# Kernel optimization log

Measured on AMD Instinct MI355X. Metric: run time of the kernel, lower is better.

## Reference

```python
import jax, jax.numpy as jnp
import numpy as np

# DNC dims: N memory slots, WM word size, R read heads, H controller hidden, D word_vec
N, WM, R, H, D = 256, 64, 4, 512, 512
T, B = 128, 32
EPS = 1e-6
IFACE = R*WM + R + WM + 1 + WM + WM + R + 1 + 1 + 3*R  # DNC interface vector size


def setup_inputs() -> dict:
    key = jax.random.key(0)
    k = jax.random.split(key, 8)
    in_dim = D + R*WM  # controller sees [x_t ; flattened read vectors]
    w = lambda kk, shape: jax.random.normal(kk, shape, jnp.float32) * 0.02
    return {
        "emb_utt": jax.random.normal(k[0], (T, B, D), jnp.float32),
        "Wx": w(k[1], (in_dim, 4*H)),
        "Wh": w(k[2], (H, 4*H)),
        "b_lstm": jnp.zeros((4*H,), jnp.float32),
        "W_pre": w(k[3], (H, D)),
        "b_pre": jnp.zeros((D,), jnp.float32),
        "W_iface": w(k[4], (H, IFACE)),
        "b_iface": jnp.zeros((IFACE,), jnp.float32),
        "W_rout": w(k[5], (R*WM, D)),
    }


def _content(M, keys, beta):
    # M: (B,N,WM); keys: (B,K,WM); beta: (B,K) -> content weighting (B,K,N)
    Mn = M / jnp.maximum(jnp.linalg.norm(M, axis=-1, keepdims=True), EPS)
    kn = keys / jnp.maximum(jnp.linalg.norm(keys, axis=-1, keepdims=True), EPS)
    sim = jnp.einsum('bkw,bnw->bkn', kn, Mn)
    return jax.nn.softmax(beta[..., None] * sim, axis=-1)


def _allocation(u):
    # usage-sort-based allocation weighting (Graves et al. 2016)
    idx = jnp.argsort(u, axis=1)  # ascending usage
    su = jnp.take_along_axis(u, idx, axis=1)
    excl = jnp.concatenate([jnp.ones_like(su[:, :1]), jnp.cumprod(su, axis=1)[:, :-1]], axis=1)
    a_sorted = (1.0 - su) * excl
    bidx = jnp.arange(u.shape[0])[:, None]
    return jnp.zeros_like(u).at[bidx, idx].set(a_sorted)


def reference(emb_utt, Wx, Wh, b_lstm, W_pre, b_pre, W_iface, b_iface, W_rout):
    Bsz = emb_utt.shape[1]
    eye = jnp.eye(N, dtype=emb_utt.dtype)

    def step(carry, x):
        h, c, M, usage, rw, ww, prec, link, rvec = carry
        # ---- controller (LSTM) ----
        xin = jnp.concatenate([x, rvec.reshape(Bsz, -1)], axis=1)
        gates = xin @ Wx + h @ Wh + b_lstm
        i, f, g, o = jnp.split(gates, 4, axis=1)
        c = jax.nn.sigmoid(f) * c + jax.nn.sigmoid(i) * jnp.tanh(g)
        h = jax.nn.sigmoid(o) * jnp.tanh(c)
        # ---- interface ----
        z = h @ W_iface + b_iface
        off = [0]
        def take(n):
            v = z[:, off[0]:off[0]+n]; off[0] += n; return v
        read_keys = take(R*WM).reshape(Bsz, R, WM)
        read_str = 1.0 + jax.nn.softplus(take(R))
        write_key = take(WM)
        write_str = 1.0 + jax.nn.softplus(take(1))
        erase = jax.nn.sigmoid(take(WM))
        write_vec = take(WM)
        free = jax.nn.sigmoid(take(R))
        alloc_g = jax.nn.sigmoid(take(1))
        write_g = jax.nn.sigmoid(take(1))
        modes = jax.nn.softmax(take(3*R).reshape(Bsz, R, 3), axis=-1)
        # ---- memory write ----
        retention = jnp.prod(1.0 - free[:, :, None] * rw, axis=1)   # (B,N)
        usage = (usage + ww - usage * ww) * retention
        alloc = _allocation(usage)
        cw = _content(M, write_key[:, None, :], write_str)[:, 0, :]  # (B,N)
        ww = write_g * (alloc_g * alloc + (1.0 - alloc_g) * cw)
        M = M * (1.0 - ww[:, :, None] * erase[:, None, :]) + ww[:, :, None] * write_vec[:, None, :]
        # temporal link matrix + precedence
        link = (1.0 - ww[:, :, None] - ww[:, None, :]) * link + ww[:, :, None] * prec[:, None, :]
        link = link * (1.0 - eye)
        prec = (1.0 - jnp.sum(ww, axis=1, keepdims=True)) * prec + ww
        # ---- memory read ----
        cr = _content(M, read_keys, read_str)                        # (B,R,N)
        fw = jnp.einsum('bij,brj->bri', link, rw)                    # forward
        bw = jnp.einsum('bji,brj->bri', link, rw)                    # backward
        rw = modes[..., 0:1] * bw + modes[..., 1:2] * cr + modes[..., 2:3] * fw
        rvec = jnp.einsum('brn,bnw->brw', rw, M)
        out = h @ W_pre + b_pre + rvec.reshape(Bsz, -1) @ W_rout
        return (h, c, M, usage, rw, ww, prec, link, rvec), out

    z = lambda *s: jnp.zeros(s, jnp.float32)
    carry0 = (z(Bsz, H), z(Bsz, H), jnp.full((Bsz, N, WM), EPS, jnp.float32),
              z(Bsz, N), z(Bsz, R, N), z(Bsz, N), z(Bsz, N),
              z(Bsz, N, N), z(Bsz, R, WM))
    _, outs = jax.lax.scan(step, carry0, emb_utt)
    return outs  # (T, B, D)
```

## Files before the change

### kernel.cpp

```cpp
#include <hip/hip_runtime.h>
#include <math.h>

#define TN   256
#define TWM  64
#define TR   4
#define TH   512
#define TD   512
#define TT   128
#define TB   32
#define IFACE 471
#define EPSI 1e-6f

#define OFF_H      0
#define OFF_C      32768
#define OFF_M      49152
#define OFF_USAGE  573440
#define OFF_RW     581632
#define OFF_WW     614400
#define OFF_PRECA  622592
#define OFF_LINK   638976
#define OFF_RVEC   2736128
#define OFF_MNORM  2744320
#define OFF_ZP     2752512
#define OFF_PARSE  2998272
#define OFF_CRS    3012608
#define OFF_FW     3045376
#define OFF_BWP    3078144
#define OFF_CNT    3340288
#define TOTAL_STATE 3340928

__device__ __forceinline__ float sigm(float x)  { return 1.0f / (1.0f + expf(-x)); }
__device__ __forceinline__ float softpl(float x){ return x > 20.0f ? x : log1pf(expf(x)); }

__device__ __forceinline__ float ldc(const float* p) {
    return __hip_atomic_load(p, __ATOMIC_RELAXED, __HIP_MEMORY_SCOPE_AGENT);
}
__device__ __forceinline__ void stc(float* p, float v) {
    __hip_atomic_store(p, v, __ATOMIC_RELAXED, __HIP_MEMORY_SCOPE_AGENT);
}
__device__ __forceinline__ void stcv4(float* p, float4 v) {
    stc(p, v.x); stc(p + 1, v.y); stc(p + 2, v.z); stc(p + 3, v.w);
}

__global__ void k_init(float* ws) {
    int idx = blockIdx.x * 256 + threadIdx.x;
    if (idx >= TOTAL_STATE) return;
    float v = 0.0f;
    if (idx >= OFF_M && idx < OFF_M + TB*TN*TWM) v = EPSI;
    if (idx >= OFF_MNORM && idx < OFF_MNORM + TB*TN) v = 8e-6f;
    ws[idx] = v;
}

__device__ __forceinline__ void out_phase(
    const float* __restrict__ W_pre, const float* __restrict__ b_pre,
    const float* __restrict__ W_rout, const float* __restrict__ ws,
    float* __restrict__ out, float* sm, const int tid, const int B2, const int t)
{
    float* act_s = sm;
    float* red_s = sm + 3072;
    const int q = B2 >> 5, s = (B2 >> 3) & 3, bg = B2 & 7, b0 = bg * 4;
    for (int i = tid; i < 768; i += 512) {
        const int bb = i / 192;
        const int k0 = (i - bb*192) * 4;
        const float* src = (k0 < 512) ? &ws[OFF_H + (t&1)*(TB*TH) + (b0+bb)*TH + k0]
                                      : &ws[OFF_RVEC + (b0+bb)*256 + (k0 - 512)];
        *(float4*)&act_s[bb*768 + k0] = *(const float4*)src;
    }
    __syncthreads();
    const int c0 = q*128 + s*32;
    const int col = tid & 31;
    const int ksb = tid >> 5;
    float a0=0, a1=0, a2=0, a3=0;
    for (int kk = ksb*48; kk < ksb*48 + 48; ++kk) {
        const float w = (kk < 512) ? W_pre[(size_t)kk * 512 + c0 + col]
                                   : W_rout[(size_t)(kk - 512) * 512 + c0 + col];
        a0 += act_s[kk]        * w;
        a1 += act_s[768 + kk]  * w;
        a2 += act_s[1536 + kk] * w;
        a3 += act_s[2304 + kk] * w;
    }
    red_s[(ksb*4 + 0)*32 + col] = a0;
    red_s[(ksb*4 + 1)*32 + col] = a1;
    red_s[(ksb*4 + 2)*32 + col] = a2;
    red_s[(ksb*4 + 3)*32 + col] = a3;
    __syncthreads();
    if (tid < 128) {
        const int cc = tid & 31, bb = tid >> 5;
        float ssum = 0.0f;
        #pragma unroll
        for (int ks2 = 0; ks2 < 16; ++ks2) ssum += red_s[(ks2*4 + bb)*32 + cc];
        ssum += b_pre[c0 + cc];
        out[(size_t)(t - 1) * (TB * TD) + (b0+bb) * TD + c0 + cc] = ssum;
    }
}

__global__ __launch_bounds__(512) void k_front(
    const float* __restrict__ emb, const float* __restrict__ Wx,
    const float* __restrict__ Wh,  const float* __restrict__ b_lstm,
    const float* __restrict__ W_pre, const float* __restrict__ b_pre,
    const float* __restrict__ W_rout,
    float* __restrict__ ws, float* __restrict__ out, int t)
{
    __shared__ __align__(16) float smem[16384];
    const int tid = threadIdx.x;
    if (blockIdx.x >= 128) {
        if (t == 0) return;
        const int raw2 = blockIdx.x - 128;
        const int B2 = (((raw2 >> 2) & 3) << 5) | ((raw2 & 3) << 3) | (raw2 >> 4);
        out_phase(W_pre, b_pre, W_rout, ws, out, smem, tid, B2, t);
        return;
    }
    if (t >= TT) return;

    const int ublk = ((blockIdx.x & 7) << 4) | (blockIdx.x >> 3);
    const int u0  = ublk * 4;
    const int cg  = tid & 3;
    const int bg  = (tid >> 2) & 7;
    const int ks  = tid >> 5;
    const int col0 = cg * 512 + u0;
    const float* hbuf = ws + OFF_H + (t & 1) * (TB * TH);

    float acc[4][4] = {};

    for (int tile = 0; tile < 5; ++tile) {
        const int T0 = tile * 256;
        {
            const int b = tid & 31, kf4 = tid >> 5;
            #pragma unroll
            for (int i = 0; i < 4; ++i) {
                const int kf = kf4 * 4 + i;
                const int kl = kf * 4;
                const int k  = T0 + kl;
                const float* src;
                if (k < 512)      src = emb + (size_t)t * (TB*TD) + b * TD + k;
                else if (k < 768) src = ws + OFF_RVEC + b * 256 + (k - 512);
                else              src = hbuf + b * TH + (k - 768);
                float4 v = *(const float4*)src;
                smem[(kl+0)*32 + b] = v.x;
                smem[(kl+1)*32 + b] = v.y;
                smem[(kl+2)*32 + b] = v.z;
                smem[(kl+3)*32 + b] = v.w;
            }
        }
        __syncthreads();
        {
            const int k0 = T0 + ks * 16;
            const float* wp = (k0 < 768 ? Wx + (size_t)k0 * 2048
                                        : Wh + (size_t)(k0 - 768) * 2048) + col0;
            const float* ap = &smem[(ks * 16) * 32 + bg * 4];
            #pragma unroll 8
            for (int kk = 0; kk < 16; ++kk) {
                float4 wv = *(const float4*)wp; wp += 2048;
                float4 av = *(const float4*)ap; ap += 32;
                acc[0][0] += wv.x*av.x; acc[0][1] += wv.x*av.y; acc[0][2] += wv.x*av.z; acc[0][3] += wv.x*av.w;
                acc[1][0] += wv.y*av.x; acc[1][1] += wv.y*av.y; acc[1][2] += wv.y*av.z; acc[1][3] += wv.y*av.w;
                acc[2][0] += wv.z*av.x; acc[2][1] += wv.z*av.y; acc[2][2] += wv.z*av.z; acc[2][3] += wv.z*av.w;
                acc[3][0] += wv.w*av.x; acc[3][1] += wv.w*av.y; acc[3][2] += wv.w*av.z; acc[3][3] += wv.w*av.w;
            }
        }
        __syncthreads();
    }

    {
        const int rbase = 8192 + ks * 512 + (cg * 8 + bg) * 16;
        *(float4*)&smem[rbase + 0]  = make_float4(acc[0][0], acc[0][1], acc[0][2], acc[0][3]);
        *(float4*)&smem[rbase + 4]  = make_float4(acc[1][0], acc[1][1], acc[1][2], acc[1][3]);
        *(float4*)&smem[rbase + 8]  = make_float4(acc[2][0], acc[2][1], acc[2][2], acc[2][3]);
        *(float4*)&smem[rbase + 12] = make_float4(acc[3][0], acc[3][1], acc[3][2], acc[3][3]);
    }
    __syncthreads();
    {
        const int o = tid;
        float s = 0.0f;
        #pragma unroll
        for (int kq = 0; kq < 16; ++kq) s += smem[8192 + kq * 512 + o];
        const int ocg = o >> 7, obg = (o >> 4) & 7, odu = (o >> 2) & 3, obb = o & 3;
        s += b_lstm[ocg * 512 + u0 + odu];
        smem[(ocg * 4 + odu) * 32 + (obg * 4 + obb)] = s;
    }
    __syncthreads();
    if (tid < 128) {
        const int du = tid >> 5, b = tid & 31;
        const float ig = smem[(0  + du) * 32 + b];
        const float fg = smem[(4  + du) * 32 + b];
        const float gg = smem[(8  + du) * 32 + b];
        const float og = smem[(12 + du) * 32 + b];
        const int ci = b * TH + u0 + du;
        const float cold = ws[OFF_C + ci];
        const float cn = sigm(fg) * cold + sigm(ig) * tanhf(gg);
        const float hn = sigm(og) * tanhf(cn);
        ws[OFF_C + ci] = cn;
        ws[OFF_H + ((t + 1) & 1) * (TB * TH) + ci] = hn;
    }
}

__device__ void stepA_fn(const float* __restrict__ b_if, float* __restrict__ ws,
                         const int t, const int b, const int tid, float* sm)
{
    float* z_s      = sm + 0;
    float* rwf_s    = sm + 480;
    float* ww_old_s = sm + 1504;
    float* ww_s     = sm + 1760;
    float* u_s      = sm + 2016;
    float* prec_s   = sm + 2272;
    float* mnorm_s  = sm + 2528;
    float* alloc_s  = sm + 2784;
    float* cw_s     = sm + 3040;
    float* keysp    = sm + 3296;
    float* wkey_s   = sm + 3552;
    float* erase_s  = sm + 3616;
    float* wvec_s   = sm + 3680;
    float* rstr_s   = sm + 3744;
    float* free_s   = sm + 3748;
    float* modesp   = sm + 3752;
    float* knorm_s  = sm + 3764;
    float* sredA_s  = sm + 3772;
    float* sc_s     = sm + 3780;
    float* Pt_s     = sm + 3788;

    const float* wsM = ws + OFF_M + b * (TN * TWM);
    const float* precOld = ws + OFF_PRECA + (t & 1) * (TB * TN) + b * 256;
    float* precNew = ws + OFF_PRECA + ((t + 1) & 1) * (TB * TN) + b * 256;

    if (tid < 256)       { *(float4*)&rwf_s[tid*4] = *(const float4*)&ws[OFF_RW + b*1024 + tid*4]; }
    else if (tid < 320)  { const int i = tid-256; *(float4*)&ww_old_s[i*4] = *(const float4*)&ws[OFF_WW + b*256 + i*4]; }
    else if (tid < 384)  { const int i = tid-320; *(float4*)&u_s[i*4]      = *(const float4*)&ws[OFF_USAGE + b*256 + i*4]; }
    else if (tid < 448)  { const int i = tid-384; *(float4*)&prec_s[i*4]   = *(const float4*)&precOld[i*4]; }
    else                 { const int i = tid-448; *(float4*)&mnorm_s[i*4]  = *(const float4*)&ws[OFF_MNORM + b*256 + i*4]; }
    if (tid < IFACE) {
        float part[16];
        #pragma unroll
        for (int p = 0; p < 16; ++p)
            part[p] = ldc(&ws[OFF_ZP + ((size_t)p*32 + b) * 480 + tid]);
        float zv = b_if[tid];
        #pragma unroll
        for (int p = 0; p < 16; ++p) zv += part[p];
        z_s[tid] = zv;
    }
    __syncthreads();

    if (tid < IFACE) {
        const float v = z_s[tid];
        if (tid < 256)       keysp[(tid >> 6)*64 + (tid & 63)] = v;
        else if (tid < 260)  rstr_s[tid - 256] = 1.0f + softpl(v);
        else if (tid < 324)  wkey_s[tid - 260] = v;
        else if (tid == 324) sc_s[0] = 1.0f + softpl(v);
        else if (tid < 389)  erase_s[tid - 325] = sigm(v);
        else if (tid < 453)  wvec_s[tid - 389] = v;
        else if (tid < 457)  free_s[tid - 453] = sigm(v);
        else if (tid == 457) sc_s[1] = sigm(v);
        else if (tid == 458) sc_s[2] = sigm(v);
    }
    __syncthreads();
    if (tid < 320) {
        const int w5 = tid >> 6, lane = tid & 63;
        const float v = (w5 == 0) ? wkey_s[lane] : keysp[(w5 - 1)*64 + lane];
        float s = v * v;
        #pragma unroll
        for (int m = 1; m <= 32; m <<= 1) s += __shfl_xor(s, m);
        if (lane == 0) knorm_s[w5] = fmaxf(sqrtf(s), EPSI);
    } else if (tid >= 508) {
        const int r = tid - 508;
        const float m0 = z_s[459 + r*3], m1 = z_s[460 + r*3], m2 = z_s[461 + r*3];
        const float mx = fmaxf(m0, fmaxf(m1, m2));
        const float e0 = expf(m0 - mx), e1 = expf(m1 - mx), e2 = expf(m2 - mx);
        const float s = e0 + e1 + e2;
        modesp[r*3+0] = e0 / s; modesp[r*3+1] = e1 / s; modesp[r*3+2] = e2 / s;
    }
    __syncthreads();

    if (tid < 404) {
        float v;
        if (tid < 256)       v = keysp[tid];
        else if (tid < 320)  v = erase_s[tid - 256];
        else if (tid < 384)  v = wvec_s[tid - 320];
        else if (tid < 388)  v = rstr_s[tid - 384];
        else if (tid < 392)  v = knorm_s[tid - 388 + 1];
        else                 v = modesp[tid - 392];
        ws[OFF_PARSE + b * 448 + tid] = v;
    }
    if (tid < 256) {
        float ret = 1.0f;
        #pragma unroll
        for (int r = 0; r < 4; ++r) ret *= 1.0f - free_s[r] * rwf_s[r*256 + tid];
        const float un = (u_s[tid] + ww_old_s[tid] - u_s[tid] * ww_old_s[tid]) * ret;
        u_s[tid] = un;
        ws[OFF_USAGE + b * 256 + tid] = un;
    }
    __syncthreads();

    {
        const int q = tid >> 8, n = tid & 255;
        const float un = u_s[n];
        float p = 1.0f;
        #pragma unroll 8
        for (int m = q * 128; m < q * 128 + 128; ++m) {
            const float um = u_s[m];
            const bool lt = (um < un) || (um == un && m < n);
            p *= lt ? um : 1.0f;
        }
        Pt_s[q * 256 + n] = p;
    }
    __syncthreads();
    if (tid < 256)
        alloc_s[tid] = (1.0f - u_s[tid]) * Pt_s[tid] * Pt_s[256 + tid];
    __syncthreads();

    {
        const int n = tid >> 1, q2 = tid & 1;
        const float* mp = wsM + n * 64 + q2 * 32;
        float s = 0.0f;
        #pragma unroll
        for (int it = 0; it < 8; ++it) {
            float4 mv = *(const float4*)(mp + it * 4);
            float4 kv = *(const float4*)&wkey_s[q2 * 32 + it * 4];
            s += mv.x*kv.x + mv.y*kv.y + mv.z*kv.z + mv.w*kv.w;
        }
        s += __shfl_xor(s, 1);
        if (q2 == 0) cw_s[n] = sc_s[0] * s / (knorm_s[0] * mnorm_s[n]);
    }
    __syncthreads();
    {
        float v = 0.0f, e = 0.0f;
        if (tid < 256) {
            v = cw_s[tid];
            float m = v;
            #pragma unroll
            for (int mm = 1; mm <= 32; mm <<= 1) m = fmaxf(m, __shfl_xor(m, mm));
            if ((tid & 63) == 0) sredA_s[tid >> 6] = m;
        }
        __syncthreads();
        if (tid == 0) sc_s[4] = fmaxf(fmaxf(sredA_s[0], sredA_s[1]), fmaxf(sredA_s[2], sredA_s[3]));
        __syncthreads();
        if (tid < 256) {
            e = expf(v - sc_s[4]);
            float s2 = e;
            #pragma unroll
            for (int mm = 1; mm <= 32; mm <<= 1) s2 += __shfl_xor(s2, mm);
            if ((tid & 63) == 0) sredA_s[tid >> 6] = s2;
        }
        __syncthreads();
        if (tid == 0) sc_s[5] = sredA_s[0] + sredA_s[1] + sredA_s[2] + sredA_s[3];
        __syncthreads();
        if (tid < 256) cw_s[tid] = e / sc_s[5];
    }
    __syncthreads();

    if (tid < 256) {
        const float wwn = sc_s[2] * (sc_s[1] * alloc_s[tid] + (1.0f - sc_s[1]) * cw_s[tid]);
        ww_s[tid] = wwn;
        ws[OFF_WW + b * 256 + tid] = wwn;
    }
    __syncthreads();
    if (tid < 256) {
        float s = ww_s[tid];
        #pragma unroll
        for (int mm = 1; mm <= 32; mm <<= 1) s += __shfl_xor(s, mm);
        if ((tid & 63) == 0) sredA_s[tid >> 6] = s;
    }
    __syncthreads();
    if (tid == 0) sc_s[3] = sredA_s[0] + sredA_s[1] + sredA_s[2] + sredA_s[3];
    __syncthreads();
    if (tid < 256)
        precNew[tid] = (1.0f - sc_s[3]) * prec_s[tid] + ww_s[tid];
}

__global__ __launch_bounds__(512) void k_zpA(
    const float* __restrict__ W_if, const float* __restrict__ b_if,
    float* __restrict__ ws, int t)
{
    __shared__ __align__(16) float h1_s[128];
    __shared__ __align__(16) float smA[4304];
    __shared__ int myBatch;
    const int tid = threadIdx.x;
    const int raw = blockIdx.x;
    const int bgz = raw >> 4;
    const int q = (raw >> 2) & 3, s = raw & 3;
    const int b0 = bgz * 4;

    if (tid < 128) {
        const int bb = tid >> 5, kk = tid & 31;
        h1_s[bb*32 + kk] = ws[OFF_H + ((t+1)&1)*(TB*TH) + (b0+bb)*TH + q*128 + s*32 + kk];
    }
    __syncthreads();
    if (tid < IFACE) {
        const int col = tid;
        float a0=0, a1=0, a2=0, a3=0;
        const float* wb = W_if + (size_t)(q*128 + s*32) * IFACE + col;
        #pragma unroll 8
        for (int kk = 0; kk < 32; ++kk) {
            const float w = *wb; wb += IFACE;
            a0 += h1_s[kk]      * w;
            a1 += h1_s[32+kk]   * w;
            a2 += h1_s[64+kk]   * w;
            a3 += h1_s[96+kk]   * w;
        }
        const size_t base = OFF_ZP + ((size_t)(q*4+s)*32 + b0) * 480 + col;
        stc(&ws[base],        a0);
        stc(&ws[base + 480],  a1);
        stc(&ws[base + 960],  a2);
        stc(&ws[base + 1440], a3);
    }
    asm volatile("s_waitcnt vmcnt(0)" ::: "memory");
    __syncthreads();
    if (tid == 0) {
        unsigned* cnt = (unsigned*)(ws + OFF_CNT) + bgz * 16;
        const unsigned old = __hip_atomic_fetch_add(cnt, 1u, __ATOMIC_RELAXED, __HIP_MEMORY_SCOPE_AGENT);
        const unsigned base = 16u * (unsigned)t;
        int mb = -1;
        if (old >= base + 12u) {
            mb = b0 + (int)(old - (base + 12u));
            while (__hip_atomic_load(cnt, __ATOMIC_RELAXED, __HIP_MEMORY_SCOPE_AGENT) < base + 16u)
                __builtin_amdgcn_s_sleep(2);
        }
        myBatch = mb;
    }
    __syncthreads();
    if (myBatch < 0) return;
    stepA_fn(b_if, ws, t, myBatch, tid, smA);
}

__device__ void stepB_fn(float* __restrict__ ws, const int t, const int b,
                         const int tid, float* sm)
{
    float* crp     = sm;
    float* rw2_s   = sm + 1024;
    float* Lt2     = sm + 2048;
    float* md      = sm + 4096;
    float* sredA_s = sm + 4112;
    float* sredB_s = sm + 4120;
    float* gmax_s  = sm + 4128;
    float* gsum_s  = sm + 4132;
    const float* wsM = ws + OFF_M + b * (TN * TWM);

    crp[tid]       = ldc(&ws[OFF_CRS + b*1024 + tid]);
    crp[tid + 512] = ldc(&ws[OFF_CRS + b*1024 + tid + 512]);
    if (tid < 12) md[tid] = ws[OFF_PARSE + b*448 + 392 + tid];
    __syncthreads();

    {
        const int rr = tid >> 8, n = tid & 255, wv = tid >> 6, lane = tid & 63;
        float v0 = crp[rr*256 + n], v1 = crp[(rr + 2)*256 + n];
        float m0 = v0, m1 = v1;
        #pragma unroll
        for (int mm = 1; mm <= 32; mm <<= 1) {
            m0 = fmaxf(m0, __shfl_xor(m0, mm));
            m1 = fmaxf(m1, __shfl_xor(m1, mm));
        }
        if (lane == 0) { sredA_s[wv] = m0; sredB_s[wv] = m1; }
        __syncthreads();
        if (tid < 4) {
            const float* base = (tid & 2) ? sredB_s : sredA_s;
            const int off = (tid & 1) * 4;
            gmax_s[tid] = fmaxf(fmaxf(base[off], base[off+1]), fmaxf(base[off+2], base[off+3]));
        }
        __syncthreads();
        const float e0 = expf(v0 - gmax_s[rr]);
        const float e1 = expf(v1 - gmax_s[rr + 2]);
        float s0 = e0, s1 = e1;
        #pragma unroll
        for (int mm = 1; mm <= 32; mm <<= 1) {
            s0 += __shfl_xor(s0, mm); s1 += __shfl_xor(s1, mm);
        }
        if (lane == 0) { sredA_s[wv] = s0; sredB_s[wv] = s1; }
        __syncthreads();
        if (tid < 4) {
            const float* base = (tid & 2) ? sredB_s : sredA_s;
            const int off = (tid & 1) * 4;
            gsum_s[tid] = base[off] + base[off+1] + base[off+2] + base[off+3];
        }
        __syncthreads();
        crp[rr*256 + n]       = e0 / gsum_s[rr];
        crp[(rr + 2)*256 + n] = e1 / gsum_s[rr + 2];
    }
    __syncthreads();

    {
        const int rr = tid >> 8, n = tid & 255;
        #pragma unroll
        for (int p = 0; p < 2; ++p) {
            const int r = rr + 2 * p;
            float part[8];
            #pragma unroll
            for (int c = 0; c < 8; ++c)
                part[c] = ldc(&ws[OFF_BWP + (size_t)(b*8 + c)*1024 + r*256 + n]);
            const float fwv = ldc(&ws[OFF_FW + b*1024 + r*256 + n]);
            float bw = 0.0f;
            #pragma unroll
            for (int c = 0; c < 8; ++c) bw += part[c];
            const float v = md[r*3] * bw + md[r*3+1] * crp[r*256 + n] + md[r*3+2] * fwv;
            rw2_s[r*256 + n] = v;
            ws[OFF_RW + b*1024 + r*256 + n] = v;
        }
    }
    __syncthreads();

    {
        const int g8 = tid >> 6, w = tid & 63;
        float p0=0, p1=0, p2=0, p3=0;
        const float* mb = wsM + (size_t)(g8 * 32) * 64 + w;
        for (int gg = 0; gg < 4; ++gg) {
            float mv[8];
            #pragma unroll
            for (int j = 0; j < 8; ++j) mv[j] = ldc(mb + (gg*8 + j) * 64);
            #pragma unroll
            for (int j = 0; j < 8; ++j) {
                const int n = g8*32 + gg*8 + j;
                p0 += rw2_s[n]       * mv[j];
                p1 += rw2_s[256 + n] * mv[j];
                p2 += rw2_s[512 + n] * mv[j];
                p3 += rw2_s[768 + n] * mv[j];
            }
        }
        Lt2[(g8*4 + 0)*64 + w] = p0;
        Lt2[(g8*4 + 1)*64 + w] = p1;
        Lt2[(g8*4 + 2)*64 + w] = p2;
        Lt2[(g8*4 + 3)*64 + w] = p3;
    }
    __syncthreads();
    if (tid < 256) {
        const int r = tid >> 6, w = tid & 63;
        float s = 0.0f;
        #pragma unroll
        for (int g = 0; g < 8; ++g) s += Lt2[(g*4 + r)*64 + w];
        ws[OFF_RVEC + b * 256 + tid] = s;
    }
}

__global__ __launch_bounds__(512) void k_linkB(float* __restrict__ ws, int t)
{
    __shared__ __align__(16) float sml[10272];
    __shared__ int isTail;
    float* ww_s   = sml;
    float* prec_s = sml + 256;
    float* rw_s   = sml + 512;
    float* pk_s   = sml + 1536;
    float* Lt     = sml + 2048;

    const int bi = blockIdx.x;
    const int b  = bi >> 3;
    const int c  = bi & 7;
    const int tid = threadIdx.x;
    const float* precOld = ws + OFF_PRECA + (t & 1) * (TB * TN) + b * 256;

    if (tid < 64)        { *(float4*)&ww_s[tid*4] = *(const float4*)&ws[OFF_WW + b*256 + tid*4]; }
    else if (tid < 128)  { const int i = tid-64;  *(float4*)&prec_s[i*4] = *(const float4*)&precOld[i*4]; }
    else if (tid < 384)  { const int i = tid-128; *(float4*)&rw_s[i*4]   = *(const float4*)&ws[OFF_RW + b*1024 + i*4]; }
    else if (tid < 496)  { const int i = tid-384; *(float4*)&pk_s[i*4]   = *(const float4*)&ws[OFF_PARSE + b*448 + i*4]; }
    __syncthreads();

    {
        const int ric = tid >> 4, c4 = (tid & 15) * 4;
        const int gi  = c * 32 + ric;
        float* mp = ws + OFF_M + b * (TN*TWM) + gi * 64 + c4;
        float4 m = *(const float4*)mp;
        const float wwi = ww_s[gi];
        float4 er = *(const float4*)&pk_s[256 + c4];
        float4 wv = *(const float4*)&pk_s[320 + c4];
        m.x = m.x * (1.0f - wwi * er.x) + wwi * wv.x;
        m.y = m.y * (1.0f - wwi * er.y) + wwi * wv.y;
        m.z = m.z * (1.0f - wwi * er.z) + wwi * wv.z;
        m.w = m.w * (1.0f - wwi * er.w) + wwi * wv.w;
        stcv4(mp, m);
        float sn = m.x*m.x + m.y*m.y + m.z*m.z + m.w*m.w;
        float d0 = m.x*pk_s[c4]     + m.y*pk_s[c4+1]     + m.z*pk_s[c4+2]     + m.w*pk_s[c4+3];
        float d1 = m.x*pk_s[64+c4]  + m.y*pk_s[64+c4+1]  + m.z*pk_s[64+c4+2]  + m.w*pk_s[64+c4+3];
        float d2 = m.x*pk_s[128+c4] + m.y*pk_s[128+c4+1] + m.z*pk_s[128+c4+2] + m.w*pk_s[128+c4+3];
        float d3 = m.x*pk_s[192+c4] + m.y*pk_s[192+c4+1] + m.z*pk_s[192+c4+2] + m.w*pk_s[192+c4+3];
        #pragma unroll
        for (int mm = 1; mm <= 8; mm <<= 1) {
            sn += __shfl_xor(sn, mm);
            d0 += __shfl_xor(d0, mm); d1 += __shfl_xor(d1, mm);
            d2 += __shfl_xor(d2, mm); d3 += __shfl_xor(d3, mm);
        }
        if ((tid & 15) == 0) {
            const float mn = fmaxf(sqrtf(sn), EPSI);
            ws[OFF_MNORM + b*256 + gi] = mn;
            const float inv = 1.0f / mn;
            stc(&ws[OFF_CRS + b*1024 + 0*256 + gi], pk_s[384+0] * d0 * inv / pk_s[388+0]);
            stc(&ws[OFF_CRS + b*1024 + 1*256 + gi], pk_s[384+1] * d1 * inv / pk_s[388+1]);
            stc(&ws[OFF_CRS + b*1024 + 2*256 + gi], pk_s[384+2] * d2 * inv / pk_s[388+2]);
            stc(&ws[OFF_CRS + b*1024 + 3*256 + gi], pk_s[384+3] * d3 * inv / pk_s[388+3]);
        }
    }

    {
        const int j = tid & 255, p = tid >> 8;
        const float wwj = ww_s[j], pj = prec_s[j];
        #pragma unroll 4
        for (int it = 0; it < 16; ++it) {
            const int ric = it * 2 + p;
            const int gi  = c * 32 + ric;
            float* lp = ws + OFF_LINK + (size_t)b * (TN*TN) + (size_t)gi * 256 + j;
            const float wwi = ww_s[gi];
            float v = (1.0f - wwi - wwj) * (*lp) + wwi * pj;
            if (j == gi) v = 0.0f;
            *lp = v;
            Lt[ric * 257 + j] = v;
        }
    }
    __syncthreads();

    {
        const int ric = tid >> 4, g = tid & 15;
        const int gi = c * 32 + ric;
        float f0=0, f1=0, f2=0, f3=0;
        #pragma unroll 4
        for (int jj = 0; jj < 16; ++jj) {
            const int j = g * 16 + jj;
            const float v = Lt[ric * 257 + j];
            f0 += v * rw_s[j]; f1 += v * rw_s[256+j];
            f2 += v * rw_s[512+j]; f3 += v * rw_s[768+j];
        }
        #pragma unroll
        for (int mm = 1; mm <= 8; mm <<= 1) {
            f0 += __shfl_xor(f0, mm); f1 += __shfl_xor(f1, mm);
            f2 += __shfl_xor(f2, mm); f3 += __shfl_xor(f3, mm);
        }
        if (g == 0) {
            stc(&ws[OFF_FW + b*1024 + gi],       f0);
            stc(&ws[OFF_FW + b*1024 + 256 + gi], f1);
            stc(&ws[OFF_FW + b*1024 + 512 + gi], f2);
            stc(&ws[OFF_FW + b*1024 + 768 + gi], f3);
        }
    }

    {
        const int j = tid & 255, p = tid >> 8;
        float b0=0, b1=0, b2=0, b3=0;
        #pragma unroll 4
        for (int it = 0; it < 16; ++it) {
            const int ric = p * 16 + it;
            const int gi  = c * 32 + ric;
            const float v = Lt[ric * 257 + j];
            b0 += v * rw_s[gi]; b1 += v * rw_s[256+gi];
            b2 += v * rw_s[512+gi]; b3 += v * rw_s[768+gi];
        }
        __syncthreads();
        if (p == 1) { Lt[j] = b0; Lt[256+j] = b1; Lt[512+j] = b2; Lt[768+j] = b3; }
        __syncthreads();
        if (p == 0) {
            stc(&ws[OFF_BWP + (size_t)bi*1024 + j],       b0 + Lt[j]);
            stc(&ws[OFF_BWP + (size_t)bi*1024 + 256 + j], b1 + Lt[256+j]);
            stc(&ws[OFF_BWP + (size_t)bi*1024 + 512 + j], b2 + Lt[512+j]);
            stc(&ws[OFF_BWP + (size_t)bi*1024 + 768 + j], b3 + Lt[768+j]);
        }
    }

    asm volatile("s_waitcnt vmcnt(0)" ::: "memory");
    __syncthreads();
    if (tid == 0) {
        unsigned* cnt = (unsigned*)(ws + OFF_CNT) + (8 + b) * 16;
        const unsigned old = __hip_atomic_fetch_add(cnt, 1u, __ATOMIC_RELAXED, __HIP_MEMORY_SCOPE_AGENT);
        isTail = (old == 8u * (unsigned)t + 7u) ? 1 : 0;
    }
    __syncthreads();
    if (!isTail) return;
    stepB_fn(ws, t, b, tid, sml);
}

extern "C" void kernel_launch(void* const* d_in, const int* in_sizes, int n_in,
                              void* d_out, int out_size, void* d_ws, size_t ws_size,
                              hipStream_t stream) {
    const float* emb    = (const float*)d_in[0];
    const float* Wx     = (const float*)d_in[1];
    const float* Wh     = (const float*)d_in[2];
    const float* b_lstm = (const float*)d_in[3];
    const float* W_pre  = (const float*)d_in[4];
    const float* b_pre  = (const float*)d_in[5];
    const float* W_if   = (const float*)d_in[6];
    const float* b_if   = (const float*)d_in[7];
    const float* W_rout = (const float*)d_in[8];
    float* out = (float*)d_out;
    float* ws  = (float*)d_ws;

    k_init<<<(TOTAL_STATE + 255) / 256, 256, 0, stream>>>(ws);
    for (int t = 0; t < TT; ++t) {
        k_front<<<256, 512, 0, stream>>>(emb, Wx, Wh, b_lstm, W_pre, b_pre, W_rout, ws, out, t);
        k_zpA<<<128, 512, 0, stream>>>(W_if, b_if, ws, t);
        k_linkB<<<256, 512, 0, stream>>>(ws, t);
    }
    k_front<<<256, 512, 0, stream>>>(emb, Wx, Wh, b_lstm, W_pre, b_pre, W_rout, ws, out, TT);
}
```

Baseline: 7.467 ms.

## Fuse interface and link kernels into one launch with per-batch flag sync

Merges the interface/stepA kernel and the link/memory-update kernel into a single 256-block kernel per timestep. Link blocks now spin on a per-batch flag that the stepA tail block sets, instead of waiting on a kernel boundary. The aim is to drop one launch per step (128 per run) and let batches proceed independently. The cost is a dependence on all 256 blocks being co-resident to avoid deadlock, plus spin-wait overhead and extra atomic loads and stores.

```diff
diff --git a/kernel.cpp b/kernel.cpp
--- a/kernel.cpp
+++ b/kernel.cpp
@@ -27,7 +27,11 @@
 #define OFF_FW     3045376
 #define OFF_BWP    3078144
 #define OFF_CNT    3340288
-#define TOTAL_STATE 3340928
+#define TOTAL_STATE 3341440
+
+#define CNT_ZPG(g) (OFF_CNT + (g)*16)
+#define CNT_SB(b)  (OFF_CNT + (8+(b))*16)
+#define CNT_FA(b)  (OFF_CNT + (40+(b))*16)
 
 __device__ __forceinline__ float sigm(float x)  { return 1.0f / (1.0f + expf(-x)); }
 __device__ __forceinline__ float softpl(float x){ return x > 20.0f ? x : log1pf(expf(x)); }
@@ -37,6 +41,11 @@
 }
 __device__ __forceinline__ void stc(float* p, float v) {
     __hip_atomic_store(p, v, __ATOMIC_RELAXED, __HIP_MEMORY_SCOPE_AGENT);
+}
+__device__ __forceinline__ float4 ldcv4(const float* p) {
+    float4 v;
+    v.x = ldc(p); v.y = ldc(p + 1); v.z = ldc(p + 2); v.w = ldc(p + 3);
+    return v;
 }
 __device__ __forceinline__ void stcv4(float* p, float4 v) {
     stc(p, v.x); stc(p + 1, v.y); stc(p + 2, v.z); stc(p + 3, v.w);
@@ -277,7 +286,7 @@
         else if (tid < 388)  v = rstr_s[tid - 384];
         else if (tid < 392)  v = knorm_s[tid - 388 + 1];
         else                 v = modesp[tid - 392];
-        ws[OFF_PARSE + b * 448 + tid] = v;
+        stc(&ws[OFF_PARSE + b * 448 + tid], v);
     }
     if (tid < 256) {
         float ret = 1.0f;
@@ -349,7 +358,7 @@
     if (tid < 256) {
         const float wwn = sc_s[2] * (sc_s[1] * alloc_s[tid] + (1.0f - sc_s[1]) * cw_s[tid]);
         ww_s[tid] = wwn;
-        ws[OFF_WW + b * 256 + tid] = wwn;
+        stc(&ws[OFF_WW + b * 256 + tid], wwn);
     }
     __syncthreads();
     if (tid < 256) {
@@ -363,61 +372,6 @@
     __syncthreads();
     if (tid < 256)
         precNew[tid] = (1.0f - sc_s[3]) * prec_s[tid] + ww_s[tid];
-}
-
-__global__ __launch_bounds__(512) void k_zpA(
-    const float* __restrict__ W_if, const float* __restrict__ b_if,
-    float* __restrict__ ws, int t)
-{
-    __shared__ __align__(16) float h1_s[128];
-    __shared__ __align__(16) float smA[4304];
-    __shared__ int myBatch;
-    const int tid = threadIdx.x;
-    const int raw = blockIdx.x;
-    const int bgz = raw >> 4;
-    const int q = (raw >> 2) & 3, s = raw & 3;
-    const int b0 = bgz * 4;
-
-    if (tid < 128) {
-        const int bb = tid >> 5, kk = tid & 31;
-        h1_s[bb*32 + kk] = ws[OFF_H + ((t+1)&1)*(TB*TH) + (b0+bb)*TH + q*128 + s*32 + kk];
-    }
-    __syncthreads();
-    if (tid < IFACE) {
-        const int col = tid;
-        float a0=0, a1=0, a2=0, a3=0;
-        const float* wb = W_if + (size_t)(q*128 + s*32) * IFACE + col;
-        #pragma unroll 8
-        for (int kk = 0; kk < 32; ++kk) {
-            const float w = *wb; wb += IFACE;
-            a0 += h1_s[kk]      * w;
-            a1 += h1_s[32+kk]   * w;
-            a2 += h1_s[64+kk]   * w;
-            a3 += h1_s[96+kk]   * w;
-        }
-        const size_t base = OFF_ZP + ((size_t)(q*4+s)*32 + b0) * 480 + col;
-        stc(&ws[base],        a0);
-        stc(&ws[base + 480],  a1);
-        stc(&ws[base + 960],  a2);
-        stc(&ws[base + 1440], a3);
-    }
-    asm volatile("s_waitcnt vmcnt(0)" ::: "memory");
-    __syncthreads();
-    if (tid == 0) {
-        unsigned* cnt = (unsigned*)(ws + OFF_CNT) + bgz * 16;
-        const unsigned old = __hip_atomic_fetch_add(cnt, 1u, __ATOMIC_RELAXED, __HIP_MEMORY_SCOPE_AGENT);
-        const unsigned base = 16u * (unsigned)t;
-        int mb = -1;
-        if (old >= base + 12u) {
-            mb = b0 + (int)(old - (base + 12u));
-            while (__hip_atomic_load(cnt, __ATOMIC_RELAXED, __HIP_MEMORY_SCOPE_AGENT) < base + 16u)
-                __builtin_amdgcn_s_sleep(2);
-        }
-        myBatch = mb;
-    }
-    __syncthreads();
-    if (myBatch < 0) return;
-    stepA_fn(b_if, ws, t, myBatch, tid, smA);
 }
 
 __device__ void stepB_fn(float* __restrict__ ws, const int t, const int b,
@@ -435,7 +389,7 @@
 
     crp[tid]       = ldc(&ws[OFF_CRS + b*1024 + tid]);
     crp[tid + 512] = ldc(&ws[OFF_CRS + b*1024 + tid + 512]);
-    if (tid < 12) md[tid] = ws[OFF_PARSE + b*448 + 392 + tid];
+    if (tid < 12) md[tid] = ldc(&ws[OFF_PARSE + b*448 + 392 + tid]);
     __syncthreads();
 
     {
@@ -527,136 +481,202 @@
     }
 }
 
-__global__ __launch_bounds__(512) void k_linkB(float* __restrict__ ws, int t)
+__global__ __launch_bounds__(512) void k_step(
+    const float* __restrict__ W_if, const float* __restrict__ b_if,
+    float* __restrict__ ws, int t)
 {
-    __shared__ __align__(16) float sml[10272];
+    __shared__ __align__(16) float sm[10272];
+    __shared__ int myBatch;
     __shared__ int isTail;
-    float* ww_s   = sml;
-    float* prec_s = sml + 256;
-    float* rw_s   = sml + 512;
-    float* pk_s   = sml + 1536;
-    float* Lt     = sml + 2048;
-
-    const int bi = blockIdx.x;
-    const int b  = bi >> 3;
-    const int c  = bi & 7;
     const int tid = threadIdx.x;
-    const float* precOld = ws + OFF_PRECA + (t & 1) * (TB * TN) + b * 256;
-
-    if (tid < 64)        { *(float4*)&ww_s[tid*4] = *(const float4*)&ws[OFF_WW + b*256 + tid*4]; }
-    else if (tid < 128)  { const int i = tid-64;  *(float4*)&prec_s[i*4] = *(const float4*)&precOld[i*4]; }
-    else if (tid < 384)  { const int i = tid-128; *(float4*)&rw_s[i*4]   = *(const float4*)&ws[OFF_RW + b*1024 + i*4]; }
-    else if (tid < 496)  { const int i = tid-384; *(float4*)&pk_s[i*4]   = *(const float4*)&ws[OFF_PARSE + b*448 + i*4]; }
-    __syncthreads();
-
-    {
-        const int ric = tid >> 4, c4 = (tid & 15) * 4;
-        const int gi  = c * 32 + ric;
-        float* mp = ws + OFF_M + b * (TN*TWM) + gi * 64 + c4;
-        float4 m = *(const float4*)mp;
-        const float wwi = ww_s[gi];
-        float4 er = *(const float4*)&pk_s[256 + c4];
-        float4 wv = *(const float4*)&pk_s[320 + c4];
-        m.x = m.x * (1.0f - wwi * er.x) + wwi * wv.x;
-        m.y = m.y * (1.0f - wwi * er.y) + wwi * wv.y;
-        m.z = m.z * (1.0f - wwi * er.z) + wwi * wv.z;
-        m.w = m.w * (1.0f - wwi * er.w) + wwi * wv.w;
-        stcv4(mp, m);
-        float sn = m.x*m.x + m.y*m.y + m.z*m.z + m.w*m.w;
-        float d0 = m.x*pk_s[c4]     + m.y*pk_s[c4+1]     + m.z*pk_s[c4+2]     + m.w*pk_s[c4+3];
-        float d1 = m.x*pk_s[64+c4]  + m.y*pk_s[64+c4+1]  + m.z*pk_s[64+c4+2]  + m.w*pk_s[64+c4+3];
-        float d2 = m.x*pk_s[128+c4] + m.y*pk_s[128+c4+1] + m.z*pk_s[128+c4+2] + m.w*pk_s[128+c4+3];
-        float d3 = m.x*pk_s[192+c4] + m.y*pk_s[192+c4+1] + m.z*pk_s[192+c4+2] + m.w*pk_s[192+c4+3];
-        #pragma unroll
-        for (int mm = 1; mm <= 8; mm <<= 1) {
-            sn += __shfl_xor(sn, mm);
-            d0 += __shfl_xor(d0, mm); d1 += __shfl_xor(d1, mm);
-            d2 += __shfl_xor(d2, mm); d3 += __shfl_xor(d3, mm);
-        }
-        if ((tid & 15) == 0) {
-            const float mn = fmaxf(sqrtf(sn), EPSI);
-            ws[OFF_MNORM + b*256 + gi] = mn;
-            const float inv = 1.0f / mn;
-            stc(&ws[OFF_CRS + b*1024 + 0*256 + gi], pk_s[384+0] * d0 * inv / pk_s[388+0]);
-            stc(&ws[OFF_CRS + b*1024 + 1*256 + gi], pk_s[384+1] * d1 * inv / pk_s[388+1]);
-            stc(&ws[OFF_CRS + b*1024 + 2*256 + gi], pk_s[384+2] * d2 * inv / pk_s[388+2]);
-            stc(&ws[OFF_CRS + b*1024 + 3*256 + gi], pk_s[384+3] * d3 * inv / pk_s[388+3]);
-        }
-    }
-
-    {
-        const int j = tid & 255, p = tid >> 8;
-        const float wwj = ww_s[j], pj = prec_s[j];
-        #pragma unroll 4
-        for (int it = 0; it < 16; ++it) {
-            const int ric = it * 2 + p;
+    const int blk = blockIdx.x;
+
+    if (blk < 128) {
+        const int bgz = blk >> 4;
+        const int q = (blk >> 2) & 3, s = blk & 3;
+        const int b0 = bgz * 4;
+        float* h1_s = sm;
+        if (tid < 128) {
+            const int bb = tid >> 5, kk = tid & 31;
+            h1_s[bb*32 + kk] = ws[OFF_H + ((t+1)&1)*(TB*TH) + (b0+bb)*TH + q*128 + s*32 + kk];
+        }
+        __syncthreads();
+        if (tid < IFACE) {
+            const int col = tid;
+            float a0=0, a1=0, a2=0, a3=0;
+            const float* wb = W_if + (size_t)(q*128 + s*32) * IFACE + col;
+            #pragma unroll 8
+            for (int kk = 0; kk < 32; ++kk) {
+                const float w = *wb; wb += IFACE;
+                a0 += h1_s[kk]      * w;
+                a1 += h1_s[32+kk]   * w;
+                a2 += h1_s[64+kk]   * w;
+                a3 += h1_s[96+kk]   * w;
+            }
+            const size_t base = OFF_ZP + ((size_t)(q*4+s)*32 + b0) * 480 + col;
+            stc(&ws[base],        a0);
+            stc(&ws[base + 480],  a1);
+            stc(&ws[base + 960],  a2);
+            stc(&ws[base + 1440], a3);
+        }
+        asm volatile("s_waitcnt vmcnt(0)" ::: "memory");
+        __syncthreads();
+        if (tid == 0) {
+            unsigned* cnt = (unsigned*)(ws + CNT_ZPG(bgz));
+            const unsigned old = __hip_atomic_fetch_add(cnt, 1u, __ATOMIC_RELAXED, __HIP_MEMORY_SCOPE_AGENT);
+            const unsigned base = 16u * (unsigned)t;
+            int mb = -1;
+            if (old >= base + 12u) {
+                mb = b0 + (int)(old - (base + 12u));
+                while (__hip_atomic_load(cnt, __ATOMIC_RELAXED, __HIP_MEMORY_SCOPE_AGENT) < base + 16u)
+                    __builtin_amdgcn_s_sleep(2);
+            }
+            myBatch = mb;
+        }
+        __syncthreads();
+        if (myBatch >= 0) {
+            stepA_fn(b_if, ws, t, myBatch, tid, sm);
+            asm volatile("s_waitcnt vmcnt(0)" ::: "memory");
+            __syncthreads();
+            if (tid == 0)
+                __hip_atomic_store((unsigned*)(ws + CNT_FA(myBatch)), (unsigned)(t + 1),
+                                   __ATOMIC_RELAXED, __HIP_MEMORY_SCOPE_AGENT);
+        }
+    }
+
+    const int b = blk >> 3;
+    const int c = blk & 7;
+    if (tid == 0) {
+        const unsigned* fa = (const unsigned*)(ws + CNT_FA(b));
+        while (__hip_atomic_load(fa, __ATOMIC_RELAXED, __HIP_MEMORY_SCOPE_AGENT) < (unsigned)(t + 1))
+            __builtin_amdgcn_s_sleep(2);
+    }
+    __syncthreads();
+    asm volatile("" ::: "memory");
+
+    {
+        float* ww_s   = sm;
+        float* prec_s = sm + 256;
+        float* rw_s   = sm + 512;
+        float* pk_s   = sm + 1536;
+        float* Lt     = sm + 2048;
+        const float* precOld = ws + OFF_PRECA + (t & 1) * (TB * TN) + b * 256;
+
+        if (tid < 64)        { *(float4*)&ww_s[tid*4] = ldcv4(&ws[OFF_WW + b*256 + tid*4]); }
+        else if (tid < 128)  { const int i = tid-64;  *(float4*)&prec_s[i*4] = *(const float4*)&precOld[i*4]; }
+        else if (tid < 384)  { const int i = tid-128; *(float4*)&rw_s[i*4]   = *(const float4*)&ws[OFF_RW + b*1024 + i*4]; }
+        else if (tid < 496)  { const int i = tid-384; *(float4*)&pk_s[i*4]   = ldcv4(&ws[OFF_PARSE + b*448 + i*4]); }
+        __syncthreads();
+
+        {
+            const int ric = tid >> 4, c4 = (tid & 15) * 4;
             const int gi  = c * 32 + ric;
-            float* lp = ws + OFF_LINK + (size_t)b * (TN*TN) + (size_t)gi * 256 + j;
+            float* mp = ws + OFF_M + b * (TN*TWM) + gi * 64 + c4;
+            float4 m = *(const float4*)mp;
             const float wwi = ww_s[gi];
-            float v = (1.0f - wwi - wwj) * (*lp) + wwi * pj;
-            if (j == gi) v = 0.0f;
-            *lp = v;
-            Lt[ric * 257 + j] = v;
-        }
-    }
-    __syncthreads();
-
-    {
-        const int ric = tid >> 4, g = tid & 15;
-        const int gi = c * 32 + ric;
-        float f0=0, f1=0, f2=0, f3=0;
-        #pragma unroll 4
-        for (int jj = 0; jj < 16; ++jj) {
-            const int j = g * 16 + jj;
-            const float v = Lt[ric * 257 + j];
-            f0 += v * rw_s[j]; f1 += v * rw_s[256+j];
-            f2 += v * rw_s[512+j]; f3 += v * rw_s[768+j];
-        }
-        #pragma unroll
-        for (int mm = 1; mm <= 8; mm <<= 1) {
-            f0 += __shfl_xor(f0, mm); f1 += __shfl_xor(f1, mm);
-            f2 += __shfl_xor(f2, mm); f3 += __shfl_xor(f3, mm);
-        }
-        if (g == 0) {
-            stc(&ws[OFF_FW + b*1024 + gi],       f0);
-            stc(&ws[OFF_FW + b*1024 + 256 + gi], f1);
-            stc(&ws[OFF_FW + b*1024 + 512 + gi], f2);
-            stc(&ws[OFF_FW + b*1024 + 768 + gi], f3);
-        }
-    }
-
-    {
-        const int j = tid & 255, p = tid >> 8;
-        float b0=0, b1=0, b2=0, b3=0;
-        #pragma unroll 4
-        for (int it = 0; it < 16; ++it) {
-            const int ric = p * 16 + it;
-            const int gi  = c * 32 + ric;
-            const float v = Lt[ric * 257 + j];
-            b0 += v * rw_s[gi]; b1 += v * rw_s[256+gi];
-            b2 += v * rw_s[512+gi]; b3 += v * rw_s[768+gi];
-        }
-        __syncthreads();
-        if (p == 1) { Lt[j] = b0; Lt[256+j] = b1; Lt[512+j] = b2; Lt[768+j] = b3; }
-        __syncthreads();
-        if (p == 0) {
-            stc(&ws[OFF_BWP + (size_t)bi*1024 + j],       b0 + Lt[j]);
-            stc(&ws[OFF_BWP + (size_t)bi*1024 + 256 + j], b1 + Lt[256+j]);
-            stc(&ws[OFF_BWP + (size_t)bi*1024 + 512 + j], b2 + Lt[512+j]);
-            stc(&ws[OFF_BWP + (size_t)bi*1024 + 768 + j], b3 + Lt[768+j]);
+            float4 er = *(const float4*)&pk_s[256 + c4];
+            float4 wv = *(const float4*)&pk_s[320 + c4];
+            m.x = m.x * (1.0f - wwi * er.x) + wwi * wv.x;
+            m.y = m.y * (1.0f - wwi * er.y) + wwi * wv.y;
+            m.z = m.z * (1.0f - wwi * er.z) + wwi * wv.z;
+            m.w = m.w * (1.0f - wwi * er.w) + wwi * wv.w;
+            stcv4(mp, m);
+            float sn = m.x*m.x + m.y*m.y + m.z*m.z + m.w*m.w;
+            float d0 = m.x*pk_s[c4]     + m.y*pk_s[c4+1]     + m.z*pk_s[c4+2]     + m.w*pk_s[c4+3];
+            float d1 = m.x*pk_s[64+c4]  + m.y*pk_s[64+c4+1]  + m.z*pk_s[64+c4+2]  + m.w*pk_s[64+c4+3];
+            float d2 = m.x*pk_s[128+c4] + m.y*pk_s[128+c4+1] + m.z*pk_s[128+c4+2] + m.w*pk_s[128+c4+3];
+            float d3 = m.x*pk_s[192+c4] + m.y*pk_s[192+c4+1] + m.z*pk_s[192+c4+2] + m.w*pk_s[192+c4+3];
+            #pragma unroll
+            for (int mm = 1; mm <= 8; mm <<= 1) {
+                sn += __shfl_xor(sn, mm);
+                d0 += __shfl_xor(d0, mm); d1 += __shfl_xor(d1, mm);
+                d2 += __shfl_xor(d2, mm); d3 += __shfl_xor(d3, mm);
+            }
+            if ((tid & 15) == 0) {
+                const float mn = fmaxf(sqrtf(sn), EPSI);
+                ws[OFF_MNORM + b*256 + gi] = mn;
+                const float inv = 1.0f / mn;
+                stc(&ws[OFF_CRS + b*1024 + 0*256 + gi], pk_s[384+0] * d0 * inv / pk_s[388+0]);
+                stc(&ws[OFF_CRS + b*1024 + 1*256 + gi], pk_s[384+1] * d1 * inv / pk_s[388+1]);
+                stc(&ws[OFF_CRS + b*1024 + 2*256 + gi], pk_s[384+2] * d2 * inv / pk_s[388+2]);
+                stc(&ws[OFF_CRS + b*1024 + 3*256 + gi], pk_s[384+3] * d3 * inv / pk_s[388+3]);
+            }
+        }
+
+        {
+            const int j = tid & 255, p = tid >> 8;
+            const float wwj = ww_s[j], pj = prec_s[j];
+            #pragma unroll 4
+            for (int it = 0; it < 16; ++it) {
+                const int ric = it * 2 + p;
+                const int gi  = c * 32 + ric;
+                float* lp = ws + OFF_LINK + (size_t)b * (TN*TN) + (size_t)gi * 256 + j;
+                const float wwi = ww_s[gi];
+                float v = (1.0f - wwi - wwj) * (*lp) + wwi * pj;
+                if (j == gi) v = 0.0f;
+                *lp = v;
+                Lt[ric * 257 + j] = v;
+            }
+        }
+        __syncthreads();
+
+        {
+            const int ric = tid >> 4, g = tid & 15;
+            const int gi = c * 32 + ric;
+            float f0=0, f1=0, f2=0, f3=0;
+            #pragma unroll 4
+            for (int jj = 0; jj < 16; ++jj) {
+                const int j = g * 16 + jj;
+                const float v = Lt[ric * 257 + j];
+                f0 += v * rw_s[j]; f1 += v * rw_s[256+j];
+                f2 += v * rw_s[512+j]; f3 += v * rw_s[768+j];
+            }
+            #pragma unroll
+            for (int mm = 1; mm <= 8; mm <<= 1) {
+                f0 += __shfl_xor(f0, mm); f1 += __shfl_xor(f1, mm);
+                f2 += __shfl_xor(f2, mm); f3 += __shfl_xor(f3, mm);
+            }
+            if (g == 0) {
+                stc(&ws[OFF_FW + b*1024 + gi],       f0);
+                stc(&ws[OFF_FW + b*1024 + 256 + gi], f1);
+                stc(&ws[OFF_FW + b*1024 + 512 + gi], f2);
+                stc(&ws[OFF_FW + b*1024 + 768 + gi], f3);
+            }
+        }
+
+        {
+            const int j = tid & 255, p = tid >> 8;
+            float b0=0, b1=0, b2=0, b3=0;
+            #pragma unroll 4
+            for (int it = 0; it < 16; ++it) {
+                const int ric = p * 16 + it;
+                const int gi  = c * 32 + ric;
+                const float v = Lt[ric * 257 + j];
+                b0 += v * rw_s[gi]; b1 += v * rw_s[256+gi];
+                b2 += v * rw_s[512+gi]; b3 += v * rw_s[768+gi];
+            }
+            __syncthreads();
+            if (p == 1) { Lt[j] = b0; Lt[256+j] = b1; Lt[512+j] = b2; Lt[768+j] = b3; }
+            __syncthreads();
+            if (p == 0) {
+                stc(&ws[OFF_BWP + (size_t)blk*1024 + j],       b0 + Lt[j]);
+                stc(&ws[OFF_BWP + (size_t)blk*1024 + 256 + j], b1 + Lt[256+j]);
+                stc(&ws[OFF_BWP + (size_t)blk*1024 + 512 + j], b2 + Lt[512+j]);
+                stc(&ws[OFF_BWP + (size_t)blk*1024 + 768 + j], b3 + Lt[768+j]);
+            }
         }
     }
 
     asm volatile("s_waitcnt vmcnt(0)" ::: "memory");
     __syncthreads();
     if (tid == 0) {
-        unsigned* cnt = (unsigned*)(ws + OFF_CNT) + (8 + b) * 16;
+        unsigned* cnt = (unsigned*)(ws + CNT_SB(b));
         const unsigned old = __hip_atomic_fetch_add(cnt, 1u, __ATOMIC_RELAXED, __HIP_MEMORY_SCOPE_AGENT);
         isTail = (old == 8u * (unsigned)t + 7u) ? 1 : 0;
     }
     __syncthreads();
     if (!isTail) return;
-    stepB_fn(ws, t, b, tid, sml);
+    stepB_fn(ws, t, b, tid, sm);
 }
 
 extern "C" void kernel_launch(void* const* d_in, const int* in_sizes, int n_in,
@@ -677,8 +697,7 @@
     k_init<<<(TOTAL_STATE + 255) / 256, 256, 0, stream>>>(ws);
     for (int t = 0; t < TT; ++t) {
         k_front<<<256, 512, 0, stream>>>(emb, Wx, Wh, b_lstm, W_pre, b_pre, W_rout, ws, out, t);
-        k_zpA<<<128, 512, 0, stream>>>(W_if, b_if, ws, t);
-        k_linkB<<<256, 512, 0, stream>>>(ws, t);
+        k_step<<<256, 512, 0, stream>>>(W_if, b_if, ws, t);
     }
     k_front<<<256, 512, 0, stream>>>(emb, Wx, Wh, b_lstm, W_pre, b_pre, W_rout, ws, out, TT);
 }
```

After: 7.305 ms. 1.02x faster.
